# Kernel tuning notes

Measured on AMD Instinct MI355X. Metric: run time of the kernel, lower is better.

Reference implementation:

```python
import jax, jax.numpy as jnp
import numpy as np

NUM_KNOTS = 64   # max(num_knots, degree+5)
DEGREE = 3
N_ROWS = 1048576

def make_knots():
    inner = np.linspace(0.0, 1.0, NUM_KNOTS - 2 * DEGREE)
    knots = np.concatenate([np.zeros(DEGREE), inner, np.ones(DEGREE)])
    return jnp.asarray(knots, dtype=jnp.float32)

def setup_inputs() -> dict:
    key = jax.random.key(0)
    x = jax.random.normal(key, (N_ROWS, 1), dtype=jnp.float32)
    return {"x": x, "knots": make_knots()}

def cox_de_boor(x, t, degree):
    # x: [N] in [0,1), t: [K] non-decreasing knots. Returns [N, K-degree-1].
    K = t.shape[0]
    # degree-0: indicator of half-open knot intervals (empty for repeated knots)
    B = ((x[:, None] >= t[None, :-1]) & (x[:, None] < t[None, 1:])).astype(x.dtype)  # [N, K-1]
    for d in range(1, degree + 1):
        m = K - 1 - d  # number of basis functions at this degree
        ld = t[d:d + m] - t[:m]            # left denominators
        rd = t[d + 1:d + 1 + m] - t[1:1 + m]  # right denominators
        left = jnp.where(ld > 0, (x[:, None] - t[None, :m]) / jnp.where(ld > 0, ld, 1.0), 0.0)
        right = jnp.where(rd > 0, (t[None, d + 1:d + 1 + m] - x[:, None]) / jnp.where(rd > 0, rd, 1.0), 0.0)
        B = left * B[:, :m] + right * B[:, 1:m + 1]
    return B  # [N, K-degree-1]

def reference(x, knots):
    xf = x.reshape(-1)
    x_min = jnp.min(xf)
    x_max = jnp.max(xf)
    # matches torch: (x - min) / (max - min + 1e-8); result strictly in [0, 1)
    xn = (xf - x_min) / (x_max - x_min + 1e-8)
    return cox_de_boor(xn, knots, DEGREE)  # [N, 60]
```

## Files before the change

kernel.cpp:

```cpp
#include <hip/hip_runtime.h>


#define N_BASIS 60

__device__ __forceinline__ float fast_rcp(float a) {
    return __builtin_amdgcn_rcpf(a);
}

__global__ __launch_bounds__(256) void k_partial_minmax(
    const float* __restrict__ x, float* __restrict__ ws, int n4) {
    const int tid = threadIdx.x;
    int gid = blockIdx.x * 256 + tid;
    const int stride = gridDim.x * 256;
    const float4* __restrict__ x4 = (const float4*)x;

    float mn = 3.4028235e38f, mx = -3.4028235e38f;
    for (int i = gid; i < n4; i += stride) {
        float4 v = x4[i];
        mn = fminf(mn, fminf(fminf(v.x, v.y), fminf(v.z, v.w)));
        mx = fmaxf(mx, fmaxf(fmaxf(v.x, v.y), fmaxf(v.z, v.w)));
    }
#pragma unroll
    for (int off = 32; off > 0; off >>= 1) {
        mn = fminf(mn, __shfl_down(mn, off, 64));
        mx = fmaxf(mx, __shfl_down(mx, off, 64));
    }
    __shared__ float smn[4], smx[4];
    if ((tid & 63) == 0) { smn[tid >> 6] = mn; smx[tid >> 6] = mx; }
    __syncthreads();
    if (tid == 0) {
        mn = fminf(fminf(smn[0], smn[1]), fminf(smn[2], smn[3]));
        mx = fmaxf(fmaxf(smx[0], smx[1]), fmaxf(smx[2], smx[3]));
        ws[blockIdx.x] = mn;
        ws[256 + blockIdx.x] = mx;
    }
}

__global__ __launch_bounds__(256) void k_final_minmax(float* __restrict__ ws) {
    const int tid = threadIdx.x;
    float mn = ws[tid];
    float mx = ws[256 + tid];
#pragma unroll
    for (int off = 32; off > 0; off >>= 1) {
        mn = fminf(mn, __shfl_down(mn, off, 64));
        mx = fmaxf(mx, __shfl_down(mx, off, 64));
    }
    __shared__ float smn[4], smx[4];
    if ((tid & 63) == 0) { smn[tid >> 6] = mn; smx[tid >> 6] = mx; }
    __syncthreads();
    if (tid == 0) {
        mn = fminf(fminf(smn[0], smn[1]), fminf(smn[2], smn[3]));
        mx = fmaxf(fmaxf(smx[0], smx[1]), fmaxf(smx[2], smx[3]));
        ws[512] = mn;
        ws[513] = (mx - mn) + 1e-8f;
    }
}

__global__ __launch_bounds__(256) void k_bspline(
    const float* __restrict__ x, const float* __restrict__ knots,
    const float* __restrict__ ws, float* __restrict__ out) {
    __shared__ float t[64];
    __shared__ float4 sN[256];
    __shared__ int sBase[256];

    const int tid = threadIdx.x;
    if (tid < 64) t[tid] = knots[tid];
    __syncthreads();

    const int row = blockIdx.x * 256 + tid;
    const float xmin = ws[512];
    const float range = ws[513];
    const float xn = (x[row] - xmin) / range;

    const bool live = (xn < 1.0f) && (xn >= 0.0f);

    int ii = (int)(xn * 57.0f);
    ii = ii < 0 ? 0 : (ii > 56 ? 56 : ii);
    int i = ii + 3;
    if (xn < t[i]) i -= 1;
    else if (xn >= t[i + 1]) i += 1;
    i = i < 3 ? 3 : (i > 59 ? 59 : i);

    const float l1 = xn - t[i];
    const float l2 = xn - t[i - 1];
    const float l3 = xn - t[i - 2];
    const float r1 = t[i + 1] - xn;
    const float r2 = t[i + 2] - xn;
    const float r3 = t[i + 3] - xn;

    float N0 = 1.0f, N1, N2, N3, temp, saved;
    temp = N0 * fast_rcp(r1 + l1);
    N0 = r1 * temp;
    N1 = l1 * temp;
    temp = N0 * fast_rcp(r1 + l2);
    N0 = r1 * temp;
    saved = l2 * temp;
    temp = N1 * fast_rcp(r2 + l1);
    N1 = saved + r2 * temp;
    N2 = l1 * temp;
    temp = N0 * fast_rcp(r1 + l3);
    N0 = r1 * temp;
    saved = l3 * temp;
    temp = N1 * fast_rcp(r2 + l2);
    N1 = saved + r2 * temp;
    saved = l2 * temp;
    temp = N2 * fast_rcp(r3 + l1);
    N2 = saved + r3 * temp;
    N3 = l1 * temp;

    const float g = live ? 1.0f : 0.0f;
    float4 Nv;
    Nv.x = N0 * g; Nv.y = N1 * g; Nv.z = N2 * g; Nv.w = N3 * g;
    sN[tid] = Nv;
    sBase[tid] = i - 3;
    __syncthreads();

    float4* __restrict__ o4 = (float4*)out + (size_t)blockIdx.x * 3840;
#pragma unroll
    for (int it = 0; it < 15; ++it) {
        const int p = tid + it * 256;
        const unsigned r = (unsigned)p / 15u;
        const int j = p - (int)r * 15;
        const float4 N = sN[r];
        const int b = sBase[r];
        const int d0 = (j << 2) - b;
        float4 v;
        v.x = (d0 == 0) ? N.x : (d0 == 1) ? N.y : (d0 == 2) ? N.z : (d0 == 3) ? N.w : 0.0f;
        const int d1 = d0 + 1;
        v.y = (d1 == 0) ? N.x : (d1 == 1) ? N.y : (d1 == 2) ? N.z : (d1 == 3) ? N.w : 0.0f;
        const int d2 = d0 + 2;
        v.z = (d2 == 0) ? N.x : (d2 == 1) ? N.y : (d2 == 2) ? N.z : (d2 == 3) ? N.w : 0.0f;
        const int d3 = d0 + 3;
        v.w = (d3 == 0) ? N.x : (d3 == 1) ? N.y : (d3 == 2) ? N.z : (d3 == 3) ? N.w : 0.0f;
        o4[p] = v;
    }
}

extern "C" void kernel_launch(void* const* d_in, const int* in_sizes, int n_in,
                              void* d_out, int out_size, void* d_ws, size_t ws_size,
                              hipStream_t stream) {
    const float* x = (const float*)d_in[0];
    const float* knots = (const float*)d_in[1];
    float* out = (float*)d_out;
    float* ws = (float*)d_ws;
    const int nrows = in_sizes[0];

    k_partial_minmax<<<256, 256, 0, stream>>>(x, ws, nrows / 4);
    k_final_minmax<<<1, 256, 0, stream>>>(ws);
    k_bspline<<<nrows / 256, 256, 0, stream>>>(x, knots, ws, out);
}
```

Measured before the change: 251.3 us.

## Fuse min/max reduction and B-spline evaluation into one cooperative kernel

Replaces the three launches (partial min/max, final min/max, B-spline expansion) with a single cooperative kernel of 512 persistent blocks that reduce min/max, synchronise the grid, and then loop over row tiles writing the 60-wide basis output. Output stores are switched to nontemporal stores. This is meant to remove the launch gaps and the extra pass between kernels, and to keep the large streaming write out of the cache. In exchange it depends on cooperative launch and a grid-wide barrier, and a fixed 512-block grid may limit occupancy during the write-bound phase.

Result: slower. 308.2 us (+22.7%).

```diff
diff --git a/kernel.cpp b/kernel.cpp
--- a/kernel.cpp
+++ b/kernel.cpp
@@ -1,138 +1,147 @@
 #include <hip/hip_runtime.h>
+#include <hip/hip_cooperative_groups.h>
+
+namespace cg = cooperative_groups;
 
 
-#define N_BASIS 60
+#define GRID 512
+#define NTHREADS 256
+
+typedef float f32x4_t __attribute__((ext_vector_type(4)));
 
 __device__ __forceinline__ float fast_rcp(float a) {
     return __builtin_amdgcn_rcpf(a);
 }
 
-__global__ __launch_bounds__(256) void k_partial_minmax(
-    const float* __restrict__ x, float* __restrict__ ws, int n4) {
-    const int tid = threadIdx.x;
-    int gid = blockIdx.x * 256 + tid;
-    const int stride = gridDim.x * 256;
-    const float4* __restrict__ x4 = (const float4*)x;
-
-    float mn = 3.4028235e38f, mx = -3.4028235e38f;
-    for (int i = gid; i < n4; i += stride) {
-        float4 v = x4[i];
-        mn = fminf(mn, fminf(fminf(v.x, v.y), fminf(v.z, v.w)));
-        mx = fmaxf(mx, fmaxf(fmaxf(v.x, v.y), fmaxf(v.z, v.w)));
-    }
-#pragma unroll
-    for (int off = 32; off > 0; off >>= 1) {
-        mn = fminf(mn, __shfl_down(mn, off, 64));
-        mx = fmaxf(mx, __shfl_down(mx, off, 64));
-    }
-    __shared__ float smn[4], smx[4];
-    if ((tid & 63) == 0) { smn[tid >> 6] = mn; smx[tid >> 6] = mx; }
-    __syncthreads();
-    if (tid == 0) {
-        mn = fminf(fminf(smn[0], smn[1]), fminf(smn[2], smn[3]));
-        mx = fmaxf(fmaxf(smx[0], smx[1]), fmaxf(smx[2], smx[3]));
-        ws[blockIdx.x] = mn;
-        ws[256 + blockIdx.x] = mx;
-    }
-}
-
-__global__ __launch_bounds__(256) void k_final_minmax(float* __restrict__ ws) {
-    const int tid = threadIdx.x;
-    float mn = ws[tid];
-    float mx = ws[256 + tid];
-#pragma unroll
-    for (int off = 32; off > 0; off >>= 1) {
-        mn = fminf(mn, __shfl_down(mn, off, 64));
-        mx = fmaxf(mx, __shfl_down(mx, off, 64));
-    }
-    __shared__ float smn[4], smx[4];
-    if ((tid & 63) == 0) { smn[tid >> 6] = mn; smx[tid >> 6] = mx; }
-    __syncthreads();
-    if (tid == 0) {
-        mn = fminf(fminf(smn[0], smn[1]), fminf(smn[2], smn[3]));
-        mx = fmaxf(fmaxf(smx[0], smx[1]), fmaxf(smx[2], smx[3]));
-        ws[512] = mn;
-        ws[513] = (mx - mn) + 1e-8f;
-    }
-}
-
-__global__ __launch_bounds__(256) void k_bspline(
+__global__ __launch_bounds__(NTHREADS, 2) void k_fused(
     const float* __restrict__ x, const float* __restrict__ knots,
-    const float* __restrict__ ws, float* __restrict__ out) {
+    float* __restrict__ ws, float* __restrict__ out, int nrows) {
     __shared__ float t[64];
     __shared__ float4 sN[256];
     __shared__ int sBase[256];
+    __shared__ float smn[4], smx[4];
+    __shared__ float sParam[2];
 
     const int tid = threadIdx.x;
+    const int bid = blockIdx.x;
     if (tid < 64) t[tid] = knots[tid];
-    __syncthreads();
 
-    const int row = blockIdx.x * 256 + tid;
-    const float xmin = ws[512];
-    const float range = ws[513];
-    const float xn = (x[row] - xmin) / range;
+    {
+        const float4* __restrict__ x4 = (const float4*)x;
+        const int n4 = nrows >> 2;
+        const int stride = GRID * NTHREADS;
+        float mn = 3.4028235e38f, mx = -3.4028235e38f;
+        for (int i = bid * NTHREADS + tid; i < n4; i += stride) {
+            float4 v = x4[i];
+            mn = fminf(mn, fminf(fminf(v.x, v.y), fminf(v.z, v.w)));
+            mx = fmaxf(mx, fmaxf(fmaxf(v.x, v.y), fmaxf(v.z, v.w)));
+        }
+#pragma unroll
+        for (int off = 32; off > 0; off >>= 1) {
+            mn = fminf(mn, __shfl_down(mn, off, 64));
+            mx = fmaxf(mx, __shfl_down(mx, off, 64));
+        }
+        if ((tid & 63) == 0) { smn[tid >> 6] = mn; smx[tid >> 6] = mx; }
+        __syncthreads();
+        if (tid == 0) {
+            mn = fminf(fminf(smn[0], smn[1]), fminf(smn[2], smn[3]));
+            mx = fmaxf(fmaxf(smx[0], smx[1]), fmaxf(smx[2], smx[3]));
+            ws[bid] = mn;
+            ws[GRID + bid] = mx;
+        }
+    }
 
-    const bool live = (xn < 1.0f) && (xn >= 0.0f);
+    cg::this_grid().sync();
 
-    int ii = (int)(xn * 57.0f);
-    ii = ii < 0 ? 0 : (ii > 56 ? 56 : ii);
-    int i = ii + 3;
-    if (xn < t[i]) i -= 1;
-    else if (xn >= t[i + 1]) i += 1;
-    i = i < 3 ? 3 : (i > 59 ? 59 : i);
+    {
+        float mn = fminf(ws[tid], ws[tid + 256]);
+        float mx = fmaxf(ws[GRID + tid], ws[GRID + tid + 256]);
+#pragma unroll
+        for (int off = 32; off > 0; off >>= 1) {
+            mn = fminf(mn, __shfl_down(mn, off, 64));
+            mx = fmaxf(mx, __shfl_down(mx, off, 64));
+        }
+        if ((tid & 63) == 0) { smn[tid >> 6] = mn; smx[tid >> 6] = mx; }
+        __syncthreads();
+        if (tid == 0) {
+            mn = fminf(fminf(smn[0], smn[1]), fminf(smn[2], smn[3]));
+            mx = fmaxf(fmaxf(smx[0], smx[1]), fmaxf(smx[2], smx[3]));
+            sParam[0] = mn;
+            sParam[1] = (mx - mn) + 1e-8f;
+        }
+        __syncthreads();
+    }
+    const float xmin = sParam[0];
+    const float range = sParam[1];
 
-    const float l1 = xn - t[i];
-    const float l2 = xn - t[i - 1];
-    const float l3 = xn - t[i - 2];
-    const float r1 = t[i + 1] - xn;
-    const float r2 = t[i + 2] - xn;
-    const float r3 = t[i + 3] - xn;
+    const int ntiles = nrows >> 8;
+    for (int tile = bid; tile < ntiles; tile += GRID) {
+        const int row = tile * 256 + tid;
+        const float xn = (x[row] - xmin) / range;
 
-    float N0 = 1.0f, N1, N2, N3, temp, saved;
-    temp = N0 * fast_rcp(r1 + l1);
-    N0 = r1 * temp;
-    N1 = l1 * temp;
-    temp = N0 * fast_rcp(r1 + l2);
-    N0 = r1 * temp;
-    saved = l2 * temp;
-    temp = N1 * fast_rcp(r2 + l1);
-    N1 = saved + r2 * temp;
-    N2 = l1 * temp;
-    temp = N0 * fast_rcp(r1 + l3);
-    N0 = r1 * temp;
-    saved = l3 * temp;
-    temp = N1 * fast_rcp(r2 + l2);
-    N1 = saved + r2 * temp;
-    saved = l2 * temp;
-    temp = N2 * fast_rcp(r3 + l1);
-    N2 = saved + r3 * temp;
-    N3 = l1 * temp;
+        const bool live = (xn < 1.0f) && (xn >= 0.0f);
 
-    const float g = live ? 1.0f : 0.0f;
-    float4 Nv;
-    Nv.x = N0 * g; Nv.y = N1 * g; Nv.z = N2 * g; Nv.w = N3 * g;
-    sN[tid] = Nv;
-    sBase[tid] = i - 3;
-    __syncthreads();
+        int ii = (int)(xn * 57.0f);
+        ii = ii < 0 ? 0 : (ii > 56 ? 56 : ii);
+        int i = ii + 3;
+        if (xn < t[i]) i -= 1;
+        else if (xn >= t[i + 1]) i += 1;
+        i = i < 3 ? 3 : (i > 59 ? 59 : i);
 
-    float4* __restrict__ o4 = (float4*)out + (size_t)blockIdx.x * 3840;
+        const float l1 = xn - t[i];
+        const float l2 = xn - t[i - 1];
+        const float l3 = xn - t[i - 2];
+        const float r1 = t[i + 1] - xn;
+        const float r2 = t[i + 2] - xn;
+        const float r3 = t[i + 3] - xn;
+
+        float N0 = 1.0f, N1, N2, N3, temp, saved;
+        temp = N0 * fast_rcp(r1 + l1);
+        N0 = r1 * temp;
+        N1 = l1 * temp;
+        temp = N0 * fast_rcp(r1 + l2);
+        N0 = r1 * temp;
+        saved = l2 * temp;
+        temp = N1 * fast_rcp(r2 + l1);
+        N1 = saved + r2 * temp;
+        N2 = l1 * temp;
+        temp = N0 * fast_rcp(r1 + l3);
+        N0 = r1 * temp;
+        saved = l3 * temp;
+        temp = N1 * fast_rcp(r2 + l2);
+        N1 = saved + r2 * temp;
+        saved = l2 * temp;
+        temp = N2 * fast_rcp(r3 + l1);
+        N2 = saved + r3 * temp;
+        N3 = l1 * temp;
+
+        const float g = live ? 1.0f : 0.0f;
+        float4 Nv;
+        Nv.x = N0 * g; Nv.y = N1 * g; Nv.z = N2 * g; Nv.w = N3 * g;
+        sN[tid] = Nv;
+        sBase[tid] = i - 3;
+        __syncthreads();
+
+        float4* __restrict__ o4 = (float4*)out + (size_t)tile * 3840;
 #pragma unroll
-    for (int it = 0; it < 15; ++it) {
-        const int p = tid + it * 256;
-        const unsigned r = (unsigned)p / 15u;
-        const int j = p - (int)r * 15;
-        const float4 N = sN[r];
-        const int b = sBase[r];
-        const int d0 = (j << 2) - b;
-        float4 v;
-        v.x = (d0 == 0) ? N.x : (d0 == 1) ? N.y : (d0 == 2) ? N.z : (d0 == 3) ? N.w : 0.0f;
-        const int d1 = d0 + 1;
-        v.y = (d1 == 0) ? N.x : (d1 == 1) ? N.y : (d1 == 2) ? N.z : (d1 == 3) ? N.w : 0.0f;
-        const int d2 = d0 + 2;
-        v.z = (d2 == 0) ? N.x : (d2 == 1) ? N.y : (d2 == 2) ? N.z : (d2 == 3) ? N.w : 0.0f;
-        const int d3 = d0 + 3;
-        v.w = (d3 == 0) ? N.x : (d3 == 1) ? N.y : (d3 == 2) ? N.z : (d3 == 3) ? N.w : 0.0f;
-        o4[p] = v;
+        for (int it = 0; it < 15; ++it) {
+            const int p = tid + it * 256;
+            const unsigned r = (unsigned)p / 15u;
+            const int j = p - (int)r * 15;
+            const float4 N = sN[r];
+            const int b = sBase[r];
+            const int d0 = (j << 2) - b;
+            float4 v;
+            v.x = (d0 == 0) ? N.x : (d0 == 1) ? N.y : (d0 == 2) ? N.z : (d0 == 3) ? N.w : 0.0f;
+            const int d1 = d0 + 1;
+            v.y = (d1 == 0) ? N.x : (d1 == 1) ? N.y : (d1 == 2) ? N.z : (d1 == 3) ? N.w : 0.0f;
+            const int d2 = d0 + 2;
+            v.z = (d2 == 0) ? N.x : (d2 == 1) ? N.y : (d2 == 2) ? N.z : (d2 == 3) ? N.w : 0.0f;
+            const int d3 = d0 + 3;
+            v.w = (d3 == 0) ? N.x : (d3 == 1) ? N.y : (d3 == 2) ? N.z : (d3 == 3) ? N.w : 0.0f;
+            __builtin_nontemporal_store(*(const f32x4_t*)&v, (f32x4_t*)&o4[p]);
+        }
+        __syncthreads();
     }
 }
 
@@ -143,9 +152,10 @@
     const float* knots = (const float*)d_in[1];
     float* out = (float*)d_out;
     float* ws = (float*)d_ws;
-    const int nrows = in_sizes[0];
+    int nrows = in_sizes[0];
 
-    k_partial_minmax<<<256, 256, 0, stream>>>(x, ws, nrows / 4);
-    k_final_minmax<<<1, 256, 0, stream>>>(ws);
-    k_bspline<<<nrows / 256, 256, 0, stream>>>(x, knots, ws, out);
+    void* args[] = {(void*)&x, (void*)&knots, (void*)&ws, (void*)&out,
+                    (void*)&nrows};
+    hipLaunchCooperativeKernel((void*)k_fused, dim3(GRID), dim3(NTHREADS),
+                               args, 0, stream);
 }
```
